# Performance work log

Hardware: AMD Instinct MI355X
Metric: run time of the kernel (lower is better)

The kernel has to match this reference:

```python
import jax, jax.numpy as jnp
import numpy as np

P, NP, EP = 10000, 50, 200      # patches, nodes/patch, edges/patch
IN, HID_E, C2, RD = 64, 256, 64, 128
HID_M, OUT, EM = 256, 16, 160000
EPS, SLOPE = 1e-5, 0.01

def lrelu(x):
    return jnp.where(x >= 0, x, SLOPE * x)

def graph_conv(x, src, dst, ew, n):
    # DGL GraphConv norm='both', bias=False, edge_weight=ew (unweighted degrees)
    ones = jnp.ones(src.shape, x.dtype)
    deg_out = jnp.maximum(jax.ops.segment_sum(ones, src, num_segments=n), 1.0)
    deg_in = jnp.maximum(jax.ops.segment_sum(ones, dst, num_segments=n), 1.0)
    h = x * jax.lax.rsqrt(deg_out)[:, None]
    agg = jax.ops.segment_sum(h[src] * ew[:, None], dst, num_segments=n)
    return agg * jax.lax.rsqrt(deg_in)[:, None]

def graph_norm(x, gamma, beta):
    # per-graph, per-channel normalization over nodes
    mu = x.mean(0, keepdims=True)
    var = x.var(0, keepdims=True)
    return gamma * (x - mu) * jax.lax.rsqrt(var + EPS) + beta

def patch_embed(feat, src, dst, ew, W1, g1, b1, W2, g2, b2, We):
    r0 = feat.mean(0)
    h = lrelu(graph_norm(graph_conv(feat, src, dst, ew, NP) @ W1, g1, b1))
    r1 = h.mean(0)
    h = lrelu(graph_norm(graph_conv(h, src, dst, ew, NP) @ W2, g2, b2))
    r2 = h.mean(0)
    return jnp.concatenate([r0, r1, r2]) @ We  # [RD]

def setup_inputs() -> dict:
    key = jax.random.key(0)
    ks = jax.random.split(key, 24)
    def kaiming(k, fi, fo):
        return jax.random.normal(k, (fi, fo), jnp.float32) * np.sqrt(2.0 / fi).astype(np.float32)
    return {
        "patch_feats": jax.random.normal(ks[0], (P, NP, IN), jnp.float32),
        "patch_src": jax.random.randint(ks[1], (P, EP), 0, NP, jnp.int32),
        "patch_dst": jax.random.randint(ks[2], (P, EP), 0, NP, jnp.int32),
        "patch_ew": jax.random.uniform(ks[3], (P, EP), jnp.float32),
        "mesh_src": jax.random.randint(ks[4], (EM,), 0, P, jnp.int32),
        "mesh_dst": jax.random.randint(ks[5], (EM,), 0, P, jnp.int32),
        "mesh_ew": jax.random.uniform(ks[6], (EM,), jnp.float32),
        "W1": kaiming(ks[7], IN, HID_E),
        "g1": 1.0 + 0.1 * jax.random.normal(ks[8], (HID_E,), jnp.float32),
        "b1": 0.1 * jax.random.normal(ks[9], (HID_E,), jnp.float32),
        "W2": kaiming(ks[10], HID_E, C2),
        "g2": 1.0 + 0.1 * jax.random.normal(ks[11], (C2,), jnp.float32),
        "b2": 0.1 * jax.random.normal(ks[12], (C2,), jnp.float32),
        "We": kaiming(ks[13], IN + HID_E + C2, RD),
        "Wc1": kaiming(ks[14], RD, HID_M),
        "g3": 1.0 + 0.1 * jax.random.normal(ks[15], (HID_M,), jnp.float32),
        "b3": 0.1 * jax.random.normal(ks[16], (HID_M,), jnp.float32),
        "Wc2": kaiming(ks[17], HID_M, HID_M),
        "g4": 1.0 + 0.1 * jax.random.normal(ks[18], (HID_M,), jnp.float32),
        "b4": 0.1 * jax.random.normal(ks[19], (HID_M,), jnp.float32),
        "Wcls": kaiming(ks[20], 2 * HID_M, OUT),
    }

def reference(patch_feats, patch_src, patch_dst, patch_ew, mesh_src, mesh_dst, mesh_ew,
              W1, g1, b1, W2, g2, b2, We, Wc1, g3, b3, Wc2, g4, b4, Wcls):
    # --- patch embedder over all patch graphs (vmapped) ---
    emb = jax.vmap(patch_embed, in_axes=(0, 0, 0, 0) + (None,) * 7)(
        patch_feats, patch_src, patch_dst, patch_ew, W1, g1, b1, W2, g2, b2, We)  # [P, RD]
    # InstanceNorm1d on 2D input == per-row normalization (no affine), then LeakyReLU
    mu = emb.mean(1, keepdims=True)
    var = emb.var(1, keepdims=True)
    emb = lrelu((emb - mu) * jax.lax.rsqrt(var + EPS))
    # --- mesh reader (single graph with P nodes) ---
    h = lrelu(graph_norm(graph_conv(emb, mesh_src, mesh_dst, mesh_ew, P) @ Wc1, g3, b3))
    ro = h.mean(0)
    h = lrelu(graph_norm(graph_conv(h, mesh_src, mesh_dst, mesh_ew, P) @ Wc2, g4, b4))
    ro = jnp.concatenate([ro, h.mean(0)])  # [2*HID_M]
    return ro[None, :] @ Wcls  # [1, OUT]
```

## Files before the change

### kernel.cpp

```cpp
#include <hip/hip_runtime.h>
#include <hip/hip_bf16.h>

#define PM    10000
#define NP_N  50
#define EP_N  200
#define EM_N  160000
#define OUT_C 16
#define EPSV  1e-5f

typedef __attribute__((ext_vector_type(8))) short short8;
typedef __attribute__((ext_vector_type(4))) float f32x4;

#define OFF_DEGO   0
#define OFF_DEGI   10016
#define OFF_OFFS   20032
#define OFF_CNT    30048
#define OFF_CUR    40064
#define OFF_CSRC   50080
#define OFF_CSRW   210080
#define OFF_STATS  370080
#define OFF_W1S    371616
#define OFF_W2S    379808
#define OFF_EMB    388000
#define OFF_AGG1   1668000
#define OFF_X1     2948000
#define OFF_HROW   5508000
#define OFF_AGG2   1668000
#define OFF_X2     4228000

__device__ __forceinline__ ushort f2bf(float f){
    __hip_bfloat16 h = __float2bfloat16(f);
    return *reinterpret_cast<ushort*>(&h);
}

__global__ __launch_bounds__(256) void prep_kernel(
    const float* __restrict__ W1, const float* __restrict__ W2,
    ushort* __restrict__ W1s, ushort* __restrict__ W2s)
{
    int gid = blockIdx.x * 256 + threadIdx.x;
    if (gid < 16384){
        int j = gid & 7, l = (gid >> 3) & 63, ki = (gid >> 9) & 1, ct = gid >> 10;
        int k = ki * 32 + ((l >> 4) << 3) + j;
        int n = ct * 16 + (l & 15);
        W1s[gid] = f2bf(W1[k * 256 + n]);
    } else {
        int g = gid - 16384;
        int j = g & 7, l = (g >> 3) & 63, ki = (g >> 9) & 7, ct = g >> 12;
        int k = ki * 32 + ((l >> 4) << 3) + j;
        int n = ct * 16 + (l & 15);
        W2s[g] = f2bf(W2[k * 64 + n]);
    }
}

__global__ __launch_bounds__(256, 4) void patch_kernel(
    const float* __restrict__ feats, const int* __restrict__ esrc,
    const int* __restrict__ edst, const float* __restrict__ eew,
    const ushort* __restrict__ W1s, const float* __restrict__ g1,
    const float* __restrict__ b1, const ushort* __restrict__ W2s,
    const float* __restrict__ g2, const float* __restrict__ b2,
    const float* __restrict__ We, float* __restrict__ embout)
{
    __shared__ __align__(16) char smem[38432];
    float*  s_A   = (float*)smem;
    char*   s_h1  = smem;
    ushort* s_fB  = (ushort*)(smem + 17408);
    ushort* s_ZB  = (ushort*)(smem + 17408);
    char*   s_G1  = smem + 25600;
    float*  s_part= (float*)(smem + 34816);
    float*  s_deg = (float*)(smem + 35840);
    float*  s_rs  = (float*)(smem + 36352);
    float*  s_r   = (float*)(smem + 36864);
    float*  s_red = (float*)(smem + 38400);

    const int tid  = threadIdx.x;
    const int p    = blockIdx.x;
    const int lane = tid & 63;
    const int wv   = tid >> 6;
    const int lnlo = lane & 15;
    const int lghi = lane >> 4;

    for (int i = tid; i < 4352; i += 256) s_A[i] = 0.f;
    for (int i = tid; i < 2048; i += 256) ((uint*)s_fB)[i] = 0u;
    if (tid < 128) s_deg[tid] = 0.f;
    int es = 0, ed = 0; float ewt = 0.f;
    if (tid < EP_N){
        es  = esrc[p * EP_N + tid];
        ed  = edst[p * EP_N + tid];
        ewt = eew[p * EP_N + tid];
    }
    __syncthreads();
    if (tid < EP_N){
        atomicAdd(&s_deg[es], 1.f);
        atomicAdd(&s_deg[64 + ed], 1.f);
        atomicAdd(&s_A[ed * 68 + es], ewt);
    }
    float4 facc = make_float4(0.f, 0.f, 0.f, 0.f);
    for (int i = tid; i < 800; i += 256){
        int s = i >> 4, cq = i & 15;
        float4 v = *(const float4*)&feats[(size_t)p * 3200 + s * 64 + cq * 4];
        facc.x += v.x; facc.y += v.y; facc.z += v.z; facc.w += v.w;
        int ki = s >> 5, ag = (s & 31) >> 3, j = s & 7;
        float vv[4] = {v.x, v.y, v.z, v.w};
        #pragma unroll
        for (int u = 0; u < 4; ++u){
            int c = cq * 4 + u;
            s_fB[(((c >> 4) * 2 + ki) * 64 + ag * 16 + (c & 15)) * 8 + j] = f2bf(vv[u]);
        }
    }
    facc.x += __shfl_xor(facc.x, 16); facc.x += __shfl_xor(facc.x, 32);
    facc.y += __shfl_xor(facc.y, 16); facc.y += __shfl_xor(facc.y, 32);
    facc.z += __shfl_xor(facc.z, 16); facc.z += __shfl_xor(facc.z, 32);
    facc.w += __shfl_xor(facc.w, 16); facc.w += __shfl_xor(facc.w, 32);
    if (lghi == 0) *(float4*)&s_part[(wv * 16 + lnlo) * 4] = facc;
    __syncthreads();
    if (tid < 128) s_rs[tid] = rsqrtf(fmaxf(s_deg[tid], 1.f));
    if (tid < 64)
        s_r[tid] = (s_part[tid] + s_part[64 + tid] + s_part[128 + tid] + s_part[192 + tid]) * 0.02f;
    __syncthreads();
    for (int i = tid; i < 4096; i += 256){
        int d = i >> 6, s = i & 63;
        s_A[d * 68 + s] *= s_rs[64 + d] * s_rs[s];
    }
    __syncthreads();
    short8 afr[4][2];
    #pragma unroll
    for (int rt = 0; rt < 4; ++rt)
        #pragma unroll
        for (int ki = 0; ki < 2; ++ki){
            int row = rt * 16 + lnlo, k0 = ki * 32 + lghi * 8;
            float4 f0 = *(const float4*)&s_A[row * 68 + k0];
            float4 f1 = *(const float4*)&s_A[row * 68 + k0 + 4];
            short8 sv;
            sv[0] = (short)f2bf(f0.x); sv[1] = (short)f2bf(f0.y);
            sv[2] = (short)f2bf(f0.z); sv[3] = (short)f2bf(f0.w);
            sv[4] = (short)f2bf(f1.x); sv[5] = (short)f2bf(f1.y);
            sv[6] = (short)f2bf(f1.z); sv[7] = (short)f2bf(f1.w);
            afr[rt][ki] = sv;
        }
    f32x4 cacc[4];
    #pragma unroll
    for (int rt = 0; rt < 4; ++rt) cacc[rt] = (f32x4){0.f, 0.f, 0.f, 0.f};
    {
        short8 fb0 = *(const short8*)&s_fB[((wv * 2 + 0) * 64 + lane) * 8];
        short8 fb1 = *(const short8*)&s_fB[((wv * 2 + 1) * 64 + lane) * 8];
        #pragma unroll
        for (int rt = 0; rt < 4; ++rt){
            cacc[rt] = __builtin_amdgcn_mfma_f32_16x16x32_bf16(afr[rt][0], fb0, cacc[rt], 0, 0, 0);
            cacc[rt] = __builtin_amdgcn_mfma_f32_16x16x32_bf16(afr[rt][1], fb1, cacc[rt], 0, 0, 0);
        }
    }
    #pragma unroll
    for (int rt = 0; rt < 4; ++rt)
        #pragma unroll
        for (int e = 0; e < 4; ++e){
            int row = rt * 16 + lghi * 4 + e;
            int col = wv * 16 + lnlo;
            *(ushort*)(s_G1 + row * 144 + ((col * 2) ^ ((row & 7) << 4))) = f2bf(cacc[rt][e]);
        }
    __syncthreads();

    f32x4 zacc[4];
    #pragma unroll
    for (int rt = 0; rt < 4; ++rt) zacc[rt] = (f32x4){0.f, 0.f, 0.f, 0.f};

    for (int h = 0; h < 2; ++h){
        short8 ga[4][2];
        #pragma unroll
        for (int rt = 0; rt < 4; ++rt)
            #pragma unroll
            for (int ki = 0; ki < 2; ++ki){
                int row = rt * 16 + lnlo, k0 = ki * 32 + lghi * 8;
                ga[rt][ki] = *(const short8*)(s_G1 + row * 144 + ((k0 * 2) ^ ((row & 7) << 4)));
            }
        #pragma unroll
        for (int ctl = 0; ctl < 2; ++ctl){
            int ctg = h * 8 + wv * 2 + ctl;
            short8 wb0 = *(const short8*)&W1s[((ctg * 2 + 0) * 64 + lane) * 8];
            short8 wb1 = *(const short8*)&W1s[((ctg * 2 + 1) * 64 + lane) * 8];
            f32x4 m[4];
            #pragma unroll
            for (int rt = 0; rt < 4; ++rt) m[rt] = (f32x4){0.f, 0.f, 0.f, 0.f};
            #pragma unroll
            for (int rt = 0; rt < 4; ++rt){
                m[rt] = __builtin_amdgcn_mfma_f32_16x16x32_bf16(ga[rt][0], wb0, m[rt], 0, 0, 0);
                m[rt] = __builtin_amdgcn_mfma_f32_16x16x32_bf16(ga[rt][1], wb1, m[rt], 0, 0, 0);
            }
            float s1 = 0.f, s2 = 0.f;
            #pragma unroll
            for (int rt = 0; rt < 4; ++rt)
                #pragma unroll
                for (int e = 0; e < 4; ++e){ float x = m[rt][e]; s1 += x; s2 += x * x; }
            s1 += __shfl_xor(s1, 16); s1 += __shfl_xor(s1, 32);
            s2 += __shfl_xor(s2, 16); s2 += __shfl_xor(s2, 32);
            float mu = s1 * 0.02f;
            float var = s2 * 0.02f - mu * mu;
            float rinv = rsqrtf(var + EPSV);
            int jg = ctg * 16 + lnlo;
            float sc = g1[jg] * rinv;
            float sh = b1[jg] - mu * sc;
            float r1p = 0.f;
            int jl = (wv * 2 + ctl) * 16 + lnlo;
            #pragma unroll
            for (int rt = 0; rt < 4; ++rt)
                #pragma unroll
                for (int e = 0; e < 4; ++e){
                    int row = rt * 16 + lghi * 4 + e;
                    float y = m[rt][e] * sc + sh;
                    float hh = (y >= 0.f) ? y : 0.01f * y;
                    hh = (row < NP_N) ? hh : 0.f;
                    r1p += hh;
                    *(ushort*)(s_h1 + row * 272 + ((jl * 2) ^ ((row & 7) << 4))) = f2bf(hh);
                }
            r1p += __shfl_xor(r1p, 16); r1p += __shfl_xor(r1p, 32);
            if (lghi == 0) s_r[64 + jg] = r1p * 0.02f;
        }
        __syncthreads();
        #pragma unroll
        for (int kil = 0; kil < 4; ++kil){
            short8 wb2 = *(const short8*)&W2s[((wv * 8 + h * 4 + kil) * 64 + lane) * 8];
            #pragma unroll
            for (int rt = 0; rt < 4; ++rt){
                int row = rt * 16 + lnlo, kl = kil * 32 + lghi * 8;
                short8 a = *(const short8*)(s_h1 + row * 272 + ((kl * 2) ^ ((row & 7) << 4)));
                zacc[rt] = __builtin_amdgcn_mfma_f32_16x16x32_bf16(a, wb2, zacc[rt], 0, 0, 0);
            }
        }
        __syncthreads();
    }

    #pragma unroll
    for (int rt = 0; rt < 4; ++rt)
        #pragma unroll
        for (int e = 0; e < 4; ++e){
            int row = rt * 16 + lghi * 4 + e;
            int ki2 = row >> 5, ag2 = (row & 31) >> 3, j2 = row & 7;
            s_ZB[((wv * 2 + ki2) * 64 + ag2 * 16 + lnlo) * 8 + j2] = f2bf(zacc[rt][e]);
        }
    __syncthreads();
    f32x4 oacc[4];
    #pragma unroll
    for (int rt = 0; rt < 4; ++rt) oacc[rt] = (f32x4){0.f, 0.f, 0.f, 0.f};
    {
        short8 zb0 = *(const short8*)&s_ZB[((wv * 2 + 0) * 64 + lane) * 8];
        short8 zb1 = *(const short8*)&s_ZB[((wv * 2 + 1) * 64 + lane) * 8];
        #pragma unroll
        for (int rt = 0; rt < 4; ++rt){
            oacc[rt] = __builtin_amdgcn_mfma_f32_16x16x32_bf16(afr[rt][0], zb0, oacc[rt], 0, 0, 0);
            oacc[rt] = __builtin_amdgcn_mfma_f32_16x16x32_bf16(afr[rt][1], zb1, oacc[rt], 0, 0, 0);
        }
    }
    {
        float s1 = 0.f, s2 = 0.f;
        #pragma unroll
        for (int rt = 0; rt < 4; ++rt)
            #pragma unroll
            for (int e = 0; e < 4; ++e){ float x = oacc[rt][e]; s1 += x; s2 += x * x; }
        s1 += __shfl_xor(s1, 16); s1 += __shfl_xor(s1, 32);
        s2 += __shfl_xor(s2, 16); s2 += __shfl_xor(s2, 32);
        float mu = s1 * 0.02f;
        float var = s2 * 0.02f - mu * mu;
        float rinv = rsqrtf(var + EPSV);
        int c2 = wv * 16 + lnlo;
        float sc = g2[c2] * rinv;
        float sh = b2[c2] - mu * sc;
        float r2p = 0.f;
        #pragma unroll
        for (int rt = 0; rt < 4; ++rt)
            #pragma unroll
            for (int e = 0; e < 4; ++e){
                int row = rt * 16 + lghi * 4 + e;
                float y = oacc[rt][e] * sc + sh;
                float hh = (y >= 0.f) ? y : 0.01f * y;
                r2p += (row < NP_N) ? hh : 0.f;
            }
        r2p += __shfl_xor(r2p, 16); r2p += __shfl_xor(r2p, 32);
        if (lghi == 0) s_r[320 + c2] = r2p * 0.02f;
    }
    __syncthreads();
    {
        int o = tid & 127, half = tid >> 7;
        float acc = 0.f;
        for (int i = half * 192; i < half * 192 + 192; ++i)
            acc = fmaf(s_r[i], We[i * 128 + o], acc);
        s_part[tid] = acc;
    }
    __syncthreads();
    float v = 0.f;
    if (tid < 128) v = s_part[tid] + s_part[tid + 128];
    float s1 = (tid < 128) ? v : 0.f;
    float s2 = s1 * s1;
    #pragma unroll
    for (int m = 32; m; m >>= 1){ s1 += __shfl_xor(s1, m); s2 += __shfl_xor(s2, m); }
    if (lane == 0 && wv < 2){ s_red[wv * 2] = s1; s_red[wv * 2 + 1] = s2; }
    __syncthreads();
    if (tid < 128){
        float T1 = s_red[0] + s_red[2], T2 = s_red[1] + s_red[3];
        float mu = T1 * (1.f / 128.f), var = T2 * (1.f / 128.f) - mu * mu;
        float y = (v - mu) * rsqrtf(var + EPSV);
        embout[(size_t)p * 128 + tid] = (y >= 0.f) ? y : 0.01f * y;
    }
}

__global__ __launch_bounds__(256) void deg_kernel(
    const int* __restrict__ msrc, const int* __restrict__ mdst,
    float* __restrict__ degO, float* __restrict__ degI, int* __restrict__ cnt)
{
    int e = blockIdx.x * 256 + threadIdx.x;
    if (e < EM_N){
        int s = msrc[e], d = mdst[e];
        atomicAdd(&degO[s], 1.f);
        atomicAdd(&degI[d], 1.f);
        atomicAdd(&cnt[d], 1);
    }
}

__global__ __launch_bounds__(256) void scan_kernel(
    const int* __restrict__ cnt, int* __restrict__ offs)
{
    __shared__ int s_sc[256];
    int t = threadIdx.x;
    int sum = 0;
    for (int k = 0; k < 40; ++k){ int i = t*40 + k; if (i < PM) sum += cnt[i]; }
    s_sc[t] = sum;
    __syncthreads();
    for (int off = 1; off < 256; off <<= 1){
        int v = (t >= off) ? s_sc[t - off] : 0;
        __syncthreads();
        s_sc[t] += v;
        __syncthreads();
    }
    int run = s_sc[t] - sum;
    for (int k = 0; k < 40; ++k){
        int i = t*40 + k;
        if (i < PM){ offs[i] = run; run += cnt[i]; }
    }
    if (t == 255) offs[PM] = s_sc[255];
}

__global__ __launch_bounds__(256) void fill_kernel(
    const int* __restrict__ msrc, const int* __restrict__ mdst,
    const float* __restrict__ mew, const float* __restrict__ degO,
    const int* __restrict__ offs, int* __restrict__ cur,
    int* __restrict__ csrc, float* __restrict__ csw)
{
    int e = blockIdx.x * 256 + threadIdx.x;
    if (e < EM_N){
        int d = mdst[e], s = msrc[e];
        int pos = atomicAdd(&cur[d], 1);
        int idx = offs[d] + pos;
        csrc[idx] = s;
        csw[idx] = mew[e] * rsqrtf(fmaxf(degO[s], 1.f));
    }
}

__global__ __launch_bounds__(256) void gather1_kernel(
    const float* __restrict__ emb, const int* __restrict__ offs,
    const int* __restrict__ csrc, const float* __restrict__ csw,
    const float* __restrict__ degI, float* __restrict__ aggT)
{
    int lane = threadIdx.x & 63, w = threadIdx.x >> 6;
    int d = blockIdx.x * 64 + lane;
    float acc[32];
    #pragma unroll
    for (int j = 0; j < 32; ++j) acc[j] = 0.f;
    if (d < PM){
        int e0 = offs[d], e1 = offs[d+1];
        for (int i = e0; i < e1; ++i){
            int s = csrc[i]; float wt = csw[i];
            const float* src = emb + (size_t)s * 128 + w * 32;
            #pragma unroll
            for (int j4 = 0; j4 < 8; ++j4){
                float4 vv = *(const float4*)(src + j4*4);
                acc[j4*4+0] = fmaf(vv.x, wt, acc[j4*4+0]);
                acc[j4*4+1] = fmaf(vv.y, wt, acc[j4*4+1]);
                acc[j4*4+2] = fmaf(vv.z, wt, acc[j4*4+2]);
                acc[j4*4+3] = fmaf(vv.w, wt, acc[j4*4+3]);
            }
        }
        float rs = rsqrtf(fmaxf(degI[d], 1.f));
        #pragma unroll
        for (int j = 0; j < 32; ++j) aggT[(size_t)(w*32 + j) * PM + d] = acc[j] * rs;
    }
}

__global__ __launch_bounds__(256) void gather2_kernel(
    const ushort* __restrict__ hRow, const int* __restrict__ offs,
    const int* __restrict__ csrc, const float* __restrict__ csw,
    const float* __restrict__ degI, float* __restrict__ aggT)
{
    int lane = threadIdx.x & 63, w = threadIdx.x >> 6;
    int d = blockIdx.x * 64 + lane;
    float acc[64];
    #pragma unroll
    for (int j = 0; j < 64; ++j) acc[j] = 0.f;
    if (d < PM){
        int e0 = offs[d], e1 = offs[d+1];
        for (int i = e0; i < e1; ++i){
            int s = csrc[i]; float wt = csw[i];
            const ushort* src = hRow + (size_t)s * 256 + w * 64;
            #pragma unroll
            for (int q4 = 0; q4 < 8; ++q4){
                uint4 qv = *(const uint4*)(src + q4*8);
                unsigned u;
                u = qv.x;
                acc[q4*8+0] = fmaf(__uint_as_float(u << 16), wt, acc[q4*8+0]);
                acc[q4*8+1] = fmaf(__uint_as_float(u & 0xffff0000u), wt, acc[q4*8+1]);
                u = qv.y;
                acc[q4*8+2] = fmaf(__uint_as_float(u << 16), wt, acc[q4*8+2]);
                acc[q4*8+3] = fmaf(__uint_as_float(u & 0xffff0000u), wt, acc[q4*8+3]);
                u = qv.z;
                acc[q4*8+4] = fmaf(__uint_as_float(u << 16), wt, acc[q4*8+4]);
                acc[q4*8+5] = fmaf(__uint_as_float(u & 0xffff0000u), wt, acc[q4*8+5]);
                u = qv.w;
                acc[q4*8+6] = fmaf(__uint_as_float(u << 16), wt, acc[q4*8+6]);
                acc[q4*8+7] = fmaf(__uint_as_float(u & 0xffff0000u), wt, acc[q4*8+7]);
            }
        }
        float rs = rsqrtf(fmaxf(degI[d], 1.f));
        #pragma unroll
        for (int j = 0; j < 64; ++j) aggT[(size_t)(w*64 + j) * PM + d] = acc[j] * rs;
    }
}

__global__ __launch_bounds__(256) void mesh_gemm_kernel(
    const float* __restrict__ AT, const float* __restrict__ W,
    float* __restrict__ XT, int K)
{
    const int tid = threadIdx.x, lane = tid & 63, wave = tid >> 6;
    const int row = blockIdx.x * 64 + lane;
    const bool act = row < PM;
    const int rowc = act ? row : (PM - 1);
    const int j0 = __builtin_amdgcn_readfirstlane((blockIdx.y * 4 + wave) * 16);
    float a[16];
    #pragma unroll
    for (int jj = 0; jj < 16; ++jj) a[jj] = 0.f;
    for (int c = 0; c < K; ++c){
        float g = AT[(size_t)c * PM + rowc];
        g = act ? g : 0.f;
        const float* wp = W + c * 256 + j0;
        #pragma unroll
        for (int jj = 0; jj < 16; ++jj) a[jj] = fmaf(g, wp[jj], a[jj]);
    }
    if (act){
        #pragma unroll
        for (int jj = 0; jj < 16; ++jj) XT[(size_t)(j0 + jj) * PM + row] = a[jj];
    }
}

__device__ __forceinline__ float block_sum2(float v1, float v2, float* s_red, float* out2)
{
    #pragma unroll
    for (int m = 32; m; m >>= 1){ v1 += __shfl_xor(v1, m); v2 += __shfl_xor(v2, m); }
    int w = threadIdx.x >> 6;
    if ((threadIdx.x & 63) == 0){ s_red[w*2] = v1; s_red[w*2+1] = v2; }
    __syncthreads();
    float t1 = s_red[0] + s_red[2] + s_red[4] + s_red[6];
    float t2 = s_red[1] + s_red[3] + s_red[5] + s_red[7];
    __syncthreads();
    *out2 = t2;
    return t1;
}

__global__ __launch_bounds__(256) void col_stats_kernel(
    const float* __restrict__ X, float* __restrict__ sums, float* __restrict__ sumsq)
{
    __shared__ float s_red[8];
    int c = blockIdx.y;
    int r = blockIdx.x * 256 + threadIdx.x;
    float v = (r < PM) ? X[(size_t)c * PM + r] : 0.f;
    float sq;
    float s = block_sum2(v, v * v, s_red, &sq);
    if (threadIdx.x == 0){ atomicAdd(&sums[c], s); atomicAdd(&sumsq[c], sq); }
}

__global__ __launch_bounds__(256) void norm1t_kernel(
    const float* __restrict__ x1T, const float* __restrict__ sums,
    const float* __restrict__ sumsq, const float* __restrict__ g,
    const float* __restrict__ b, float* __restrict__ ro, ushort* __restrict__ hRow)
{
    __shared__ float s_tile[64][65];
    int lane = threadIdx.x & 63, wvv = threadIdx.x >> 6;
    int cg = blockIdx.y;
    int rb = blockIdx.x * 64;
    int r = rb + lane;
    for (int cc = wvv; cc < 64; cc += 4){
        int c = cg * 64 + cc;
        float mu = sums[c] * (1.f / PM);
// ... 7 lines not shown
            h = (y >= 0.f) ? y : 0.01f * y;
        }
        s_tile[cc][lane] = h;
        float t = h;
        #pragma unroll
        for (int m = 32; m; m >>= 1) t += __shfl_xor(t, m);
        if (lane == 0) atomicAdd(&ro[c], t);
    }
    __syncthreads();
    for (int i = wvv; i < 64; i += 4){
        int rr = rb + i;
        if (rr < PM) hRow[(size_t)rr * 256 + cg * 64 + lane] = f2bf(s_tile[i][lane]);
    }
}

__global__ __launch_bounds__(256) void norm2_kernel(
    const float* __restrict__ X, const float* __restrict__ sums,
    const float* __restrict__ sumsq, const float* __restrict__ g,
    const float* __restrict__ b, float* __restrict__ ro)
{
    __shared__ float s_red[8];
    int c = blockIdx.y;
    int r = blockIdx.x * 256 + threadIdx.x;
    float mu = sums[c] * (1.f / PM);
    float var = sumsq[c] * (1.f / PM) - mu * mu;
    float sc = g[c] * rsqrtf(var + EPSV);
    float h = 0.f;
    if (r < PM){
        float x = X[(size_t)c * PM + r];
        float y = sc * (x - mu) + b[c];
        h = (y >= 0.f) ? y : 0.01f * y;
    }
    float dummy;
    float s = block_sum2(h, 0.f, s_red, &dummy);
    if (threadIdx.x == 0) atomicAdd(&ro[c], s);
}

__global__ __launch_bounds__(256) void final_kernel(
    const float* __restrict__ ro, const float* __restrict__ Wcls,
    float* __restrict__ out)
{
    __shared__ float s_part[256];
    int tid = threadIdx.x;
    int o = tid & 15, seg = tid >> 4;
    float pacc = 0.f;
    for (int j = seg * 32; j < seg * 32 + 32; ++j)
        pacc = fmaf(ro[j] * (1.f / PM), Wcls[j * OUT_C + o], pacc);
    s_part[tid] = pacc;
    __syncthreads();
// ... 23 lines not shown
    const float* b2    = (const float*)d_in[12];
    const float* We    = (const float*)d_in[13];
    const float* Wc1   = (const float*)d_in[14];
    const float* g3    = (const float*)d_in[15];
    const float* b3    = (const float*)d_in[16];
    const float* Wc2   = (const float*)d_in[17];
    const float* g4    = (const float*)d_in[18];
    const float* b4    = (const float*)d_in[19];
    const float* Wcls  = (const float*)d_in[20];
    float* out = (float*)d_out;
    float* ws  = (float*)d_ws;

    float*  degO  = ws + OFF_DEGO;
    float*  degI  = ws + OFF_DEGI;
    int*    offs  = (int*)(ws + OFF_OFFS);
    int*    cnt   = (int*)(ws + OFF_CNT);
    int*    cur   = (int*)(ws + OFF_CUR);
    int*    csrc  = (int*)(ws + OFF_CSRC);
    float*  csw   = ws + OFF_CSRW;
    float*  sums1 = ws + OFF_STATS;
    float*  sumsq1= ws + OFF_STATS + 256;
    float*  sums2 = ws + OFF_STATS + 512;
    float*  sumsq2= ws + OFF_STATS + 768;
    float*  ro    = ws + OFF_STATS + 1024;
    ushort* W1s   = (ushort*)(ws + OFF_W1S);
    ushort* W2s   = (ushort*)(ws + OFF_W2S);
    float*  emb   = ws + OFF_EMB;
    float*  agg1T = ws + OFF_AGG1;
    float*  x1T   = ws + OFF_X1;
    ushort* hRow  = (ushort*)(ws + OFF_HROW);
    float*  agg2T = ws + OFF_AGG2;
    float*  x2T   = ws + OFF_X2;

    hipMemsetAsync(degO, 0, 20032 * sizeof(float), stream);
    hipMemsetAsync(cnt,  0, 10016 * sizeof(int), stream);
    hipMemsetAsync(cur,  0, 10016 * sizeof(int), stream);
    hipMemsetAsync(sums1,0, 1536 * sizeof(float), stream);

    prep_kernel<<<128, 256, 0, stream>>>(W1, W2, W1s, W2s);
    patch_kernel<<<PM, 256, 0, stream>>>(feats, psrc, pdst, pew,
                                         W1s, g1, b1, W2s, g2, b2, We, emb);
    deg_kernel<<<EM_N/256, 256, 0, stream>>>(msrc, mdst, degO, degI, cnt);
    scan_kernel<<<1, 256, 0, stream>>>(cnt, offs);
    fill_kernel<<<EM_N/256, 256, 0, stream>>>(msrc, mdst, mew, degO, offs, cur, csrc, csw);
    gather1_kernel<<<157, 256, 0, stream>>>(emb, offs, csrc, csw, degI, agg1T);
    mesh_gemm_kernel<<<dim3(157, 4), 256, 0, stream>>>(agg1T, Wc1, x1T, 128);
    col_stats_kernel<<<dim3(40, 256), 256, 0, stream>>>(x1T, sums1, sumsq1);
    norm1t_kernel<<<dim3(157, 4), 256, 0, stream>>>(x1T, sums1, sumsq1, g3, b3, ro, hRow);
    gather2_kernel<<<157, 256, 0, stream>>>(hRow, offs, csrc, csw, degI, agg2T);
    mesh_gemm_kernel<<<dim3(157, 4), 256, 0, stream>>>(agg2T, Wc2, x2T, 256);
    col_stats_kernel<<<dim3(40, 256), 256, 0, stream>>>(x2T, sums2, sumsq2);
    norm2_kernel<<<dim3(40, 256), 256, 0, stream>>>(x2T, sums2, sumsq2, g4, b4, ro + 256);
    final_kernel<<<1, 256, 0, stream>>>(ro, Wcls, out);
}
```

Before: 926.6 us.

## Restructure patch kernel and fuse mesh gather, GEMM and column stats

The patch kernel now loads features straight into registers as MFMA B-fragments, folds degree normalisation into the edge atomics, and swaps the LDS round trip for Z with lane shuffles. It also drops the per-block We projection, using less shared memory so five blocks can fit per CU. The readout projection and instance norm move to a new batched emb_kernel. In the mesh stage, gather, GEMM and column-stat reduction are fused into ggemm kernels, and the separate count array is dropped in favour of the in-degree, cutting several launches and intermediate buffers. The risk is that the fused kernels run a scalar fp32 GEMM with more stat atomics, and the workspace layout now aliases more buffers.

```diff
diff --git a/kernel.cpp b/kernel.cpp
--- a/kernel.cpp
+++ b/kernel.cpp
@@ -14,23 +14,22 @@
 #define OFF_DEGO   0
 #define OFF_DEGI   10016
 #define OFF_OFFS   20032
-#define OFF_CNT    30048
-#define OFF_CUR    40064
-#define OFF_CSRC   50080
-#define OFF_CSRW   210080
-#define OFF_STATS  370080
-#define OFF_W1S    371616
-#define OFF_W2S    379808
-#define OFF_EMB    388000
-#define OFF_AGG1   1668000
-#define OFF_X1     2948000
-#define OFF_HROW   5508000
-#define OFF_AGG2   1668000
-#define OFF_X2     4228000
+#define OFF_CUR    30048
+#define OFF_CSRC   40064
+#define OFF_CSRW   200064
+#define OFF_STATS  360064
+#define OFF_W1S    361600
+#define OFF_W2S    369792
+#define OFF_RBUF   377984
+#define OFF_EMB    4217984
+#define OFF_X1T    5497984
 
 __device__ __forceinline__ ushort f2bf(float f){
     __hip_bfloat16 h = __float2bfloat16(f);
     return *reinterpret_cast<ushort*>(&h);
+}
+__device__ __forceinline__ uint pack2(float a, float b){
+    return (uint)f2bf(a) | ((uint)f2bf(b) << 16);
 }
 
 __global__ __launch_bounds__(256) void prep_kernel(
@@ -52,25 +51,21 @@
     }
 }
 
-__global__ __launch_bounds__(256, 4) void patch_kernel(
+__global__ __launch_bounds__(256, 5) void patch_kernel(
     const float* __restrict__ feats, const int* __restrict__ esrc,
     const int* __restrict__ edst, const float* __restrict__ eew,
     const ushort* __restrict__ W1s, const float* __restrict__ g1,
     const float* __restrict__ b1, const ushort* __restrict__ W2s,
     const float* __restrict__ g2, const float* __restrict__ b2,
-    const float* __restrict__ We, float* __restrict__ embout)
-{
-    __shared__ __align__(16) char smem[38432];
-    float*  s_A   = (float*)smem;
-    char*   s_h1  = smem;
-    ushort* s_fB  = (ushort*)(smem + 17408);
-    ushort* s_ZB  = (ushort*)(smem + 17408);
-    char*   s_G1  = smem + 25600;
-    float*  s_part= (float*)(smem + 34816);
-    float*  s_deg = (float*)(smem + 35840);
-    float*  s_rs  = (float*)(smem + 36352);
-    float*  s_r   = (float*)(smem + 36864);
-    float*  s_red = (float*)(smem + 38400);
+    float* __restrict__ rbuf)
+{
+    __shared__ __align__(16) char smem[29184];
+    float* s_A  = (float*)smem;
+    char*  s_h1 = smem;
+    char*  s_G1 = smem + 17408;
+    float* s_deg = (float*)(smem + 26624);
+    float* s_rs  = (float*)(smem + 27136);
+    float* s_r   = (float*)(smem + 27648);
 
     const int tid  = threadIdx.x;
     const int p    = blockIdx.x;
@@ -79,48 +74,51 @@
     const int lnlo = lane & 15;
     const int lghi = lane >> 4;
 
-    for (int i = tid; i < 4352; i += 256) s_A[i] = 0.f;
-    for (int i = tid; i < 2048; i += 256) ((uint*)s_fB)[i] = 0u;
-    if (tid < 128) s_deg[tid] = 0.f;
+    float fl[2][8];
+    {
+        const float* fbase = feats + (size_t)p * 3200 + wv * 16 + lnlo;
+        #pragma unroll
+        for (int ki = 0; ki < 2; ++ki)
+            #pragma unroll
+            for (int j = 0; j < 8; ++j){
+                int s = ki * 32 + lghi * 8 + j;
+                int sc = (s < NP_N) ? s : (NP_N - 1);
+                fl[ki][j] = fbase[sc * 64];
+            }
+    }
     int es = 0, ed = 0; float ewt = 0.f;
     if (tid < EP_N){
         es  = esrc[p * EP_N + tid];
         ed  = edst[p * EP_N + tid];
         ewt = eew[p * EP_N + tid];
     }
+    for (int i = tid; i < 1088; i += 256)
+        *(float4*)&s_A[i * 4] = make_float4(0.f, 0.f, 0.f, 0.f);
+    if (tid < 128) s_deg[tid] = 0.f;
     __syncthreads();
     if (tid < EP_N){
         atomicAdd(&s_deg[es], 1.f);
         atomicAdd(&s_deg[64 + ed], 1.f);
-        atomicAdd(&s_A[ed * 68 + es], ewt);
-    }
-    float4 facc = make_float4(0.f, 0.f, 0.f, 0.f);
-    for (int i = tid; i < 800; i += 256){
-        int s = i >> 4, cq = i & 15;
-        float4 v = *(const float4*)&feats[(size_t)p * 3200 + s * 64 + cq * 4];
-        facc.x += v.x; facc.y += v.y; facc.z += v.z; facc.w += v.w;
-        int ki = s >> 5, ag = (s & 31) >> 3, j = s & 7;
-        float vv[4] = {v.x, v.y, v.z, v.w};
-        #pragma unroll
-        for (int u = 0; u < 4; ++u){
-            int c = cq * 4 + u;
-            s_fB[(((c >> 4) * 2 + ki) * 64 + ag * 16 + (c & 15)) * 8 + j] = f2bf(vv[u]);
-        }
-    }
-    facc.x += __shfl_xor(facc.x, 16); facc.x += __shfl_xor(facc.x, 32);
-    facc.y += __shfl_xor(facc.y, 16); facc.y += __shfl_xor(facc.y, 32);
-    facc.z += __shfl_xor(facc.z, 16); facc.z += __shfl_xor(facc.z, 32);
-    facc.w += __shfl_xor(facc.w, 16); facc.w += __shfl_xor(facc.w, 32);
-    if (lghi == 0) *(float4*)&s_part[(wv * 16 + lnlo) * 4] = facc;
+    }
+    float r0s = 0.f;
+    #pragma unroll
+    for (int ki = 0; ki < 2; ++ki)
+        #pragma unroll
+        for (int j = 0; j < 8; ++j)
+            r0s += (ki * 32 + lghi * 8 + j < NP_N) ? fl[ki][j] : 0.f;
+    r0s += __shfl_xor(r0s, 16); r0s += __shfl_xor(r0s, 32);
     __syncthreads();
     if (tid < 128) s_rs[tid] = rsqrtf(fmaxf(s_deg[tid], 1.f));
-    if (tid < 64)
-        s_r[tid] = (s_part[tid] + s_part[64 + tid] + s_part[128 + tid] + s_part[192 + tid]) * 0.02f;
-    __syncthreads();
-    for (int i = tid; i < 4096; i += 256){
-        int d = i >> 6, s = i & 63;
-        s_A[d * 68 + s] *= s_rs[64 + d] * s_rs[s];
-    }
+    if (lghi == 0) s_r[wv * 16 + lnlo] = r0s * 0.02f;
+    short8 fbf[2];
+    #pragma unroll
+    for (int ki = 0; ki < 2; ++ki)
+        #pragma unroll
+        for (int j = 0; j < 8; ++j)
+            fbf[ki][j] = (short)f2bf(fl[ki][j]);
+    __syncthreads();
+    if (tid < EP_N)
+        atomicAdd(&s_A[ed * 68 + es], ewt * s_rs[es] * s_rs[64 + ed]);
     __syncthreads();
     short8 afr[4][2];
     #pragma unroll
@@ -139,15 +137,11 @@
         }
     f32x4 cacc[4];
     #pragma unroll
-    for (int rt = 0; rt < 4; ++rt) cacc[rt] = (f32x4){0.f, 0.f, 0.f, 0.f};
-    {
-        short8 fb0 = *(const short8*)&s_fB[((wv * 2 + 0) * 64 + lane) * 8];
-        short8 fb1 = *(const short8*)&s_fB[((wv * 2 + 1) * 64 + lane) * 8];
-        #pragma unroll
-        for (int rt = 0; rt < 4; ++rt){
-            cacc[rt] = __builtin_amdgcn_mfma_f32_16x16x32_bf16(afr[rt][0], fb0, cacc[rt], 0, 0, 0);
-            cacc[rt] = __builtin_amdgcn_mfma_f32_16x16x32_bf16(afr[rt][1], fb1, cacc[rt], 0, 0, 0);
-        }
+    for (int rt = 0; rt < 4; ++rt) cacc[rt] = (f32x4){0.f,0.f,0.f,0.f};
+    #pragma unroll
+    for (int rt = 0; rt < 4; ++rt){
+        cacc[rt] = __builtin_amdgcn_mfma_f32_16x16x32_bf16(afr[rt][0], fbf[0], cacc[rt], 0,0,0);
+        cacc[rt] = __builtin_amdgcn_mfma_f32_16x16x32_bf16(afr[rt][1], fbf[1], cacc[rt], 0,0,0);
     }
     #pragma unroll
     for (int rt = 0; rt < 4; ++rt)
@@ -155,13 +149,13 @@
         for (int e = 0; e < 4; ++e){
             int row = rt * 16 + lghi * 4 + e;
             int col = wv * 16 + lnlo;
-            *(ushort*)(s_G1 + row * 144 + ((col * 2) ^ ((row & 7) << 4))) = f2bf(cacc[rt][e]);
+            *(ushort*)(s_G1 + row * 144 + ((col * 2) ^ ((row & 8) << 2))) = f2bf(cacc[rt][e]);
         }
     __syncthreads();
 
     f32x4 zacc[4];
     #pragma unroll
-    for (int rt = 0; rt < 4; ++rt) zacc[rt] = (f32x4){0.f, 0.f, 0.f, 0.f};
+    for (int rt = 0; rt < 4; ++rt) zacc[rt] = (f32x4){0.f,0.f,0.f,0.f};
 
     for (int h = 0; h < 2; ++h){
         short8 ga[4][2];
@@ -170,7 +164,7 @@
             #pragma unroll
             for (int ki = 0; ki < 2; ++ki){
                 int row = rt * 16 + lnlo, k0 = ki * 32 + lghi * 8;
-                ga[rt][ki] = *(const short8*)(s_G1 + row * 144 + ((k0 * 2) ^ ((row & 7) << 4)));
+                ga[rt][ki] = *(const short8*)(s_G1 + row * 144 + ((k0 * 2) ^ ((row & 8) << 2)));
             }
         #pragma unroll
         for (int ctl = 0; ctl < 2; ++ctl){
@@ -179,17 +173,17 @@
             short8 wb1 = *(const short8*)&W1s[((ctg * 2 + 1) * 64 + lane) * 8];
             f32x4 m[4];
             #pragma unroll
-            for (int rt = 0; rt < 4; ++rt) m[rt] = (f32x4){0.f, 0.f, 0.f, 0.f};
+            for (int rt = 0; rt < 4; ++rt) m[rt] = (f32x4){0.f,0.f,0.f,0.f};
             #pragma unroll
             for (int rt = 0; rt < 4; ++rt){
-                m[rt] = __builtin_amdgcn_mfma_f32_16x16x32_bf16(ga[rt][0], wb0, m[rt], 0, 0, 0);
-                m[rt] = __builtin_amdgcn_mfma_f32_16x16x32_bf16(ga[rt][1], wb1, m[rt], 0, 0, 0);
+                m[rt] = __builtin_amdgcn_mfma_f32_16x16x32_bf16(ga[rt][0], wb0, m[rt], 0,0,0);
+                m[rt] = __builtin_amdgcn_mfma_f32_16x16x32_bf16(ga[rt][1], wb1, m[rt], 0,0,0);
             }
             float s1 = 0.f, s2 = 0.f;
             #pragma unroll
             for (int rt = 0; rt < 4; ++rt)
                 #pragma unroll
-                for (int e = 0; e < 4; ++e){ float x = m[rt][e]; s1 += x; s2 += x * x; }
+                for (int e = 0; e < 4; ++e){ float x = m[rt][e]; s1 += x; s2 += x*x; }
             s1 += __shfl_xor(s1, 16); s1 += __shfl_xor(s1, 32);
             s2 += __shfl_xor(s2, 16); s2 += __shfl_xor(s2, 32);
             float mu = s1 * 0.02f;
@@ -209,7 +203,7 @@
                     float hh = (y >= 0.f) ? y : 0.01f * y;
                     hh = (row < NP_N) ? hh : 0.f;
                     r1p += hh;
-                    *(ushort*)(s_h1 + row * 272 + ((jl * 2) ^ ((row & 7) << 4))) = f2bf(hh);
+                    *(ushort*)(s_h1 + row * 272 + ((jl * 2) ^ ((row & 8) << 2))) = f2bf(hh);
                 }
             r1p += __shfl_xor(r1p, 16); r1p += __shfl_xor(r1p, 32);
             if (lghi == 0) s_r[64 + jg] = r1p * 0.02f;
@@ -221,40 +215,52 @@
             #pragma unroll
             for (int rt = 0; rt < 4; ++rt){
                 int row = rt * 16 + lnlo, kl = kil * 32 + lghi * 8;
-                short8 a = *(const short8*)(s_h1 + row * 272 + ((kl * 2) ^ ((row & 7) << 4)));
-                zacc[rt] = __builtin_amdgcn_mfma_f32_16x16x32_bf16(a, wb2, zacc[rt], 0, 0, 0);
+                short8 a = *(const short8*)(s_h1 + row * 272 + ((kl * 2) ^ ((row & 8) << 2)));
+                zacc[rt] = __builtin_amdgcn_mfma_f32_16x16x32_bf16(a, wb2, zacc[rt], 0,0,0);
             }
         }
         __syncthreads();
     }
 
-    #pragma unroll
-    for (int rt = 0; rt < 4; ++rt)
-        #pragma unroll
-        for (int e = 0; e < 4; ++e){
-            int row = rt * 16 + lghi * 4 + e;
-            int ki2 = row >> 5, ag2 = (row & 31) >> 3, j2 = row & 7;
-            s_ZB[((wv * 2 + ki2) * 64 + ag2 * 16 + lnlo) * 8 + j2] = f2bf(zacc[rt][e]);
-        }
-    __syncthreads();
+    uint pk[4][2];
+    #pragma unroll
+    for (int rt = 0; rt < 4; ++rt){
+        pk[rt][0] = pack2(zacc[rt][0], zacc[rt][1]);
+        pk[rt][1] = pack2(zacc[rt][2], zacc[rt][3]);
+    }
+    bool hi = (lghi >= 2);
+    int lane_lo = (((lghi * 2 + 0) & 3) << 4) + lnlo;
+    int lane_hi = (((lghi * 2 + 1) & 3) << 4) + lnlo;
+    short8 zb[2];
+    #pragma unroll
+    for (int ki = 0; ki < 2; ++ki){
+        uint sA = hi ? pk[ki*2+1][0] : pk[ki*2][0];
+        uint sB = hi ? pk[ki*2+1][1] : pk[ki*2][1];
+        uint w0 = (uint)__shfl((int)sA, lane_lo, 64);
+        uint w1 = (uint)__shfl((int)sB, lane_lo, 64);
+        uint w2 = (uint)__shfl((int)sA, lane_hi, 64);
+        uint w3 = (uint)__shfl((int)sB, lane_hi, 64);
+        short8 z;
+        z[0] = (short)(w0 & 0xffff); z[1] = (short)(w0 >> 16);
+        z[2] = (short)(w1 & 0xffff); z[3] = (short)(w1 >> 16);
+        z[4] = (short)(w2 & 0xffff); z[5] = (short)(w2 >> 16);
+        z[6] = (short)(w3 & 0xffff); z[7] = (short)(w3 >> 16);
+        zb[ki] = z;
+    }
     f32x4 oacc[4];
     #pragma unroll
-    for (int rt = 0; rt < 4; ++rt) oacc[rt] = (f32x4){0.f, 0.f, 0.f, 0.f};
-    {
-        short8 zb0 = *(const short8*)&s_ZB[((wv * 2 + 0) * 64 + lane) * 8];
-        short8 zb1 = *(const short8*)&s_ZB[((wv * 2 + 1) * 64 + lane) * 8];
-        #pragma unroll
-        for (int rt = 0; rt < 4; ++rt){
-            oacc[rt] = __builtin_amdgcn_mfma_f32_16x16x32_bf16(afr[rt][0], zb0, oacc[rt], 0, 0, 0);
-            oacc[rt] = __builtin_amdgcn_mfma_f32_16x16x32_bf16(afr[rt][1], zb1, oacc[rt], 0, 0, 0);
-        }
+    for (int rt = 0; rt < 4; ++rt) oacc[rt] = (f32x4){0.f,0.f,0.f,0.f};
+    #pragma unroll
+    for (int rt = 0; rt < 4; ++rt){
+        oacc[rt] = __builtin_amdgcn_mfma_f32_16x16x32_bf16(afr[rt][0], zb[0], oacc[rt], 0,0,0);
+        oacc[rt] = __builtin_amdgcn_mfma_f32_16x16x32_bf16(afr[rt][1], zb[1], oacc[rt], 0,0,0);
     }
     {
         float s1 = 0.f, s2 = 0.f;
         #pragma unroll
         for (int rt = 0; rt < 4; ++rt)
             #pragma unroll
-            for (int e = 0; e < 4; ++e){ float x = oacc[rt][e]; s1 += x; s2 += x * x; }
+            for (int e = 0; e < 4; ++e){ float x = oacc[rt][e]; s1 += x; s2 += x*x; }
         s1 += __shfl_xor(s1, 16); s1 += __shfl_xor(s1, 32);
         s2 += __shfl_xor(s2, 16); s2 += __shfl_xor(s2, 32);
         float mu = s1 * 0.02f;
@@ -277,50 +283,72 @@
         if (lghi == 0) s_r[320 + c2] = r2p * 0.02f;
     }
     __syncthreads();
-    {
-        int o = tid & 127, half = tid >> 7;
-        float acc = 0.f;
-        for (int i = half * 192; i < half * 192 + 192; ++i)
-            acc = fmaf(s_r[i], We[i * 128 + o], acc);
-        s_part[tid] = acc;
-    }
-    __syncthreads();
-    float v = 0.f;
-    if (tid < 128) v = s_part[tid] + s_part[tid + 128];
-    float s1 = (tid < 128) ? v : 0.f;
-    float s2 = s1 * s1;
-    #pragma unroll
-    for (int m = 32; m; m >>= 1){ s1 += __shfl_xor(s1, m); s2 += __shfl_xor(s2, m); }
-    if (lane == 0 && wv < 2){ s_red[wv * 2] = s1; s_red[wv * 2 + 1] = s2; }
-    __syncthreads();
-    if (tid < 128){
-        float T1 = s_red[0] + s_red[2], T2 = s_red[1] + s_red[3];
-        float mu = T1 * (1.f / 128.f), var = T2 * (1.f / 128.f) - mu * mu;
-        float y = (v - mu) * rsqrtf(var + EPSV);
-        embout[(size_t)p * 128 + tid] = (y >= 0.f) ? y : 0.01f * y;
-    }
+    if (tid < 96)
+        *(float4*)&rbuf[(size_t)p * 384 + tid * 4] = *(const float4*)&s_r[tid * 4];
+}
+
+__global__ __launch_bounds__(256) void emb_kernel(
+    const float* __restrict__ rbuf, const float* __restrict__ We,
+    float* __restrict__ emb)
+{
+    __shared__ float s_R[16 * 388];
+    int tid = threadIdx.x;
+    int rb = blockIdx.x * 16;
+    for (int i = tid; i < 1536; i += 256){
+        int r = i / 96, q = i - r * 96;
+        *(float4*)&s_R[r * 388 + q * 4] =
+            *(const float4*)&rbuf[(size_t)(rb + r) * 384 + q * 4];
+    }
+    __syncthreads();
+    int r = tid >> 4, c0 = (tid & 15) * 8;
+    float acc[8];
+    #pragma unroll
+    for (int j = 0; j < 8; ++j) acc[j] = 0.f;
+    for (int k = 0; k < 384; ++k){
+        float a = s_R[r * 388 + k];
+        const float* wp = &We[k * 128 + c0];
+        #pragma unroll
+        for (int j = 0; j < 8; ++j) acc[j] = fmaf(a, wp[j], acc[j]);
+    }
+    float s1 = 0.f, s2 = 0.f;
+    #pragma unroll
+    for (int j = 0; j < 8; ++j){ s1 += acc[j]; s2 += acc[j] * acc[j]; }
+    s1 += __shfl_xor(s1, 1); s2 += __shfl_xor(s2, 1);
+    s1 += __shfl_xor(s1, 2); s2 += __shfl_xor(s2, 2);
+    s1 += __shfl_xor(s1, 4); s2 += __shfl_xor(s2, 4);
+    s1 += __shfl_xor(s1, 8); s2 += __shfl_xor(s2, 8);
+    float mu = s1 * (1.f / 128.f);
+    float var = s2 * (1.f / 128.f) - mu * mu;
+    float rinv = rsqrtf(var + EPSV);
+    float o[8];
+    #pragma unroll
+    for (int j = 0; j < 8; ++j){
+        float y = (acc[j] - mu) * rinv;
+        o[j] = (y >= 0.f) ? y : 0.01f * y;
+    }
+    float* op = &emb[(size_t)(rb + r) * 128 + c0];
+    *(float4*)op = make_float4(o[0], o[1], o[2], o[3]);
+    *(float4*)(op + 4) = make_float4(o[4], o[5], o[6], o[7]);
 }
 
 __global__ __launch_bounds__(256) void deg_kernel(
     const int* __restrict__ msrc, const int* __restrict__ mdst,
-    float* __restrict__ degO, float* __restrict__ degI, int* __restrict__ cnt)
+    float* __restrict__ degO, float* __restrict__ degI)
 {
     int e = blockIdx.x * 256 + threadIdx.x;
     if (e < EM_N){
-        int s = msrc[e], d = mdst[e];
-        atomicAdd(&degO[s], 1.f);
-        atomicAdd(&degI[d], 1.f);
-        atomicAdd(&cnt[d], 1);
+        atomicAdd(&degO[msrc[e]], 1.f);
+        atomicAdd(&degI[mdst[e]], 1.f);
     }
 }
 
 __global__ __launch_bounds__(256) void scan_kernel(
-    const int* __restrict__ cnt, int* __restrict__ offs)
+    const float* __restrict__ degI, int* __restrict__ offs)
 {
     __shared__ int s_sc[256];
     int t = threadIdx.x;
     int sum = 0;
-    for (int k = 0; k < 40; ++k){ int i = t*40 + k; if (i < PM) sum += cnt[i]; }
+    for (int k = 0; k < 40; ++k){ int i = t * 40 + k; if (i < PM) sum += (int)degI[i]; }
     s_sc[t] = sum;
     __syncthreads();
     for (int off = 1; off < 256; off <<= 1){
@@ -331,8 +359,8 @@
     }
     int run = s_sc[t] - sum;
     for (int k = 0; k < 40; ++k){
-        int i = t*40 + k;
-        if (i < PM){ offs[i] = run; run += cnt[i]; }
+        int i = t * 40 + k;
+        if (i < PM){ offs[i] = run; run += (int)degI[i]; }
     }
     if (t == 255) offs[PM] = s_sc[255];
 }
@@ -353,124 +381,65 @@
     }
 }
 
-__global__ __launch_bounds__(256) void gather1_kernel(
+__global__ __launch_bounds__(256) void ggemm1_kernel(
     const float* __restrict__ emb, const int* __restrict__ offs,
     const int* __restrict__ csrc, const float* __restrict__ csw,
-    const float* __restrict__ degI, float* __restrict__ aggT)
-{
-    int lane = threadIdx.x & 63, w = threadIdx.x >> 6;
-    int d = blockIdx.x * 64 + lane;
-    float acc[32];
-    #pragma unroll
-    for (int j = 0; j < 32; ++j) acc[j] = 0.f;
-    if (d < PM){
-        int e0 = offs[d], e1 = offs[d+1];
-        for (int i = e0; i < e1; ++i){
-            int s = csrc[i]; float wt = csw[i];
-            const float* src = emb + (size_t)s * 128 + w * 32;
-            #pragma unroll
-            for (int j4 = 0; j4 < 8; ++j4){
-                float4 vv = *(const float4*)(src + j4*4);
-                acc[j4*4+0] = fmaf(vv.x, wt, acc[j4*4+0]);
-                acc[j4*4+1] = fmaf(vv.y, wt, acc[j4*4+1]);
-                acc[j4*4+2] = fmaf(vv.z, wt, acc[j4*4+2]);
-                acc[j4*4+3] = fmaf(vv.w, wt, acc[j4*4+3]);
-            }
+    const float* __restrict__ degI, const float* __restrict__ Wc1,
+    float* __restrict__ x1T, float* __restrict__ sums, float* __restrict__ sumsq)
+{
+    __shared__ float s_agg[16 * 132];
+    int tid = threadIdx.x, lane = tid & 63, w = tid >> 6;
+    for (int i = 0; i < 4; ++i){
+        int li = w * 4 + i;
+        int d = blockIdx.x * 16 + li;
+        int e0 = offs[d], e1 = offs[d + 1];
+        float a0 = 0.f, a1 = 0.f;
+        int e = e0;
+        for (; e + 1 < e1; e += 2){
+            int sA = csrc[e], sB = csrc[e + 1];
+            float wA = csw[e], wB = csw[e + 1];
+            float2 vA = *(const float2*)&emb[(size_t)sA * 128 + lane * 2];
+            float2 vB = *(const float2*)&emb[(size_t)sB * 128 + lane * 2];
+            a0 = fmaf(vA.x, wA, a0); a1 = fmaf(vA.y, wA, a1);
+            a0 = fmaf(vB.x, wB, a0); a1 = fmaf(vB.y, wB, a1);
+        }
+        if (e < e1){
+            int sA = csrc[e]; float wA = csw[e];
+            float2 vA = *(const float2*)&emb[(size_t)sA * 128 + lane * 2];
+            a0 = fmaf(vA.x, wA, a0); a1 = fmaf(vA.y, wA, a1);
         }
         float rs = rsqrtf(fmaxf(degI[d], 1.f));
-        #pragma unroll
-        for (int j = 0; j < 32; ++j) aggT[(size_t)(w*32 + j) * PM + d] = acc[j] * rs;
-    }
-}
-
-__global__ __launch_bounds__(256) void gather2_kernel(
-    const ushort* __restrict__ hRow, const int* __restrict__ offs,
-    const int* __restrict__ csrc, const float* __restrict__ csw,
-    const float* __restrict__ degI, float* __restrict__ aggT)
-{
-    int lane = threadIdx.x & 63, w = threadIdx.x >> 6;
-    int d = blockIdx.x * 64 + lane;
-    float acc[64];
-    #pragma unroll
-    for (int j = 0; j < 64; ++j) acc[j] = 0.f;
-    if (d < PM){
-        int e0 = offs[d], e1 = offs[d+1];
-        for (int i = e0; i < e1; ++i){
-            int s = csrc[i]; float wt = csw[i];
-            const ushort* src = hRow + (size_t)s * 256 + w * 64;
-            #pragma unroll
-            for (int q4 = 0; q4 < 8; ++q4){
-                uint4 qv = *(const uint4*)(src + q4*8);
-                unsigned u;
-                u = qv.x;
-                acc[q4*8+0] = fmaf(__uint_as_float(u << 16), wt, acc[q4*8+0]);
-                acc[q4*8+1] = fmaf(__uint_as_float(u & 0xffff0000u), wt, acc[q4*8+1]);
-                u = qv.y;
-                acc[q4*8+2] = fmaf(__uint_as_float(u << 16), wt, acc[q4*8+2]);
-                acc[q4*8+3] = fmaf(__uint_as_float(u & 0xffff0000u), wt, acc[q4*8+3]);
-                u = qv.z;
-                acc[q4*8+4] = fmaf(__uint_as_float(u << 16), wt, acc[q4*8+4]);
-                acc[q4*8+5] = fmaf(__uint_as_float(u & 0xffff0000u), wt, acc[q4*8+5]);
-                u = qv.w;
-                acc[q4*8+6] = fmaf(__uint_as_float(u << 16), wt, acc[q4*8+6]);
-                acc[q4*8+7] = fmaf(__uint_as_float(u & 0xffff0000u), wt, acc[q4*8+7]);
-            }
-        }
-        float rs = rsqrtf(fmaxf(degI[d], 1.f));
-        #pragma unroll
-        for (int j = 0; j < 64; ++j) aggT[(size_t)(w*64 + j) * PM + d] = acc[j] * rs;
-    }
-}
-
-__global__ __launch_bounds__(256) void mesh_gemm_kernel(
-    const float* __restrict__ AT, const float* __restrict__ W,
-    float* __restrict__ XT, int K)
-{
-    const int tid = threadIdx.x, lane = tid & 63, wave = tid >> 6;
-    const int row = blockIdx.x * 64 + lane;
-    const bool act = row < PM;
-    const int rowc = act ? row : (PM - 1);
-    const int j0 = __builtin_amdgcn_readfirstlane((blockIdx.y * 4 + wave) * 16);
-    float a[16];
-    #pragma unroll
-    for (int jj = 0; jj < 16; ++jj) a[jj] = 0.f;
-    for (int c = 0; c < K; ++c){
-        float g = AT[(size_t)c * PM + rowc];
-        g = act ? g : 0.f;
-        const float* wp = W + c * 256 + j0;
-        #pragma unroll
-        for (int jj = 0; jj < 16; ++jj) a[jj] = fmaf(g, wp[jj], a[jj]);
-    }
-    if (act){
-        #pragma unroll
-        for (int jj = 0; jj < 16; ++jj) XT[(size_t)(j0 + jj) * PM + row] = a[jj];
-    }
-}
-
-__device__ __forceinline__ float block_sum2(float v1, float v2, float* s_red, float* out2)
-{
-    #pragma unroll
-    for (int m = 32; m; m >>= 1){ v1 += __shfl_xor(v1, m); v2 += __shfl_xor(v2, m); }
-    int w = threadIdx.x >> 6;
-    if ((threadIdx.x & 63) == 0){ s_red[w*2] = v1; s_red[w*2+1] = v2; }
-    __syncthreads();
-    float t1 = s_red[0] + s_red[2] + s_red[4] + s_red[6];
-    float t2 = s_red[1] + s_red[3] + s_red[5] + s_red[7];
-    __syncthreads();
-    *out2 = t2;
-    return t1;
-}
-
-__global__ __launch_bounds__(256) void col_stats_kernel(
-    const float* __restrict__ X, float* __restrict__ sums, float* __restrict__ sumsq)
-{
-    __shared__ float s_red[8];
-    int c = blockIdx.y;
-    int r = blockIdx.x * 256 + threadIdx.x;
-    float v = (r < PM) ? X[(size_t)c * PM + r] : 0.f;
-    float sq;
-    float s = block_sum2(v, v * v, s_red, &sq);
-    if (threadIdx.x == 0){ atomicAdd(&sums[c], s); atomicAdd(&sumsq[c], sq); }
+        s_agg[li * 132 + lane * 2]     = a0 * rs;
+        s_agg[li * 132 + lane * 2 + 1] = a1 * rs;
+    }
+    __syncthreads();
+    int r = lane & 15, cg = lane >> 4;
+    int c0 = w * 64 + cg * 16;
+    float acc[16];
+    #pragma unroll
+    for (int jj = 0; jj < 16; ++jj) acc[jj] = 0.f;
+    #pragma unroll 2
+    for (int k = 0; k < 128; ++k){
+        float a = s_agg[r * 132 + k];
+        const float* wp = &Wc1[k * 256 + c0];
+        #pragma unroll
+        for (int jj = 0; jj < 16; ++jj) acc[jj] = fmaf(a, wp[jj], acc[jj]);
+    }
+    int row = blockIdx.x * 16 + r;
+    #pragma unroll
+    for (int jj = 0; jj < 16; ++jj) x1T[(size_t)(c0 + jj) * PM + row] = acc[jj];
+    #pragma unroll
+    for (int jj = 0; jj < 16; ++jj){
+        float s1 = acc[jj], s2 = acc[jj] * acc[jj];
+        s1 += __shfl_xor(s1, 1); s2 += __shfl_xor(s2, 1);
+        s1 += __shfl_xor(s1, 2); s2 += __shfl_xor(s2, 2);
+        s1 += __shfl_xor(s1, 4); s2 += __shfl_xor(s2, 4);
+        s1 += __shfl_xor(s1, 8); s2 += __shfl_xor(s2, 8);
+        if (r == 0){
+            atomicAdd(&sums[c0 + jj], s1);
+            atomicAdd(&sumsq[c0 + jj], s2);
+        }
+    }
 }
 
 __global__ __launch_bounds__(256) void norm1t_kernel(
@@ -508,12 +477,79 @@
     }
 }
 
+__global__ __launch_bounds__(256) void ggemm2_kernel(
+    const ushort* __restrict__ hRow, const int* __restrict__ offs,
+    const int* __restrict__ csrc, const float* __restrict__ csw,
+    const float* __restrict__ degI, const float* __restrict__ Wc2,
+    float* __restrict__ x2T, float* __restrict__ sums, float* __restrict__ sumsq)
+{
+    __shared__ float s_agg[16 * 260];
+    int tid = threadIdx.x, lane = tid & 63, w = tid >> 6;
+    for (int i = 0; i < 4; ++i){
+        int li = w * 4 + i;
+        int d = blockIdx.x * 16 + li;
+        int e0 = offs[d], e1 = offs[d + 1];
+        float a0 = 0.f, a1 = 0.f, a2 = 0.f, a3 = 0.f;
+        for (int e = e0; e < e1; ++e){
+            int s = csrc[e]; float wt = csw[e];
+            uint2 qv = *(const uint2*)&hRow[(size_t)s * 256 + lane * 4];
+            a0 = fmaf(__uint_as_float(qv.x << 16), wt, a0);
+            a1 = fmaf(__uint_as_float(qv.x & 0xffff0000u), wt, a1);
+            a2 = fmaf(__uint_as_float(qv.y << 16), wt, a2);
+            a3 = fmaf(__uint_as_float(qv.y & 0xffff0000u), wt, a3);
+        }
+        float rs = rsqrtf(fmaxf(degI[d], 1.f));
+        *(float4*)&s_agg[li * 260 + lane * 4] =
+            make_float4(a0 * rs, a1 * rs, a2 * rs, a3 * rs);
+    }
+    __syncthreads();
+    int r = lane & 15, cg = lane >> 4;
+    int c0 = w * 64 + cg * 16;
+    float acc[16];
+    #pragma unroll
+    for (int jj = 0; jj < 16; ++jj) acc[jj] = 0.f;
+    #pragma unroll 2
+    for (int k = 0; k < 256; ++k){
+        float a = s_agg[r * 260 + k];
+        const float* wp = &Wc2[k * 256 + c0];
+        #pragma unroll
+        for (int jj = 0; jj < 16; ++jj) acc[jj] = fmaf(a, wp[jj], acc[jj]);
+    }
+    int row = blockIdx.x * 16 + r;
+    #pragma unroll
+    for (int jj = 0; jj < 16; ++jj) x2T[(size_t)(c0 + jj) * PM + row] = acc[jj];
+    #pragma unroll
+    for (int jj = 0; jj < 16; ++jj){
+        float s1 = acc[jj], s2 = acc[jj] * acc[jj];
+        s1 += __shfl_xor(s1, 1); s2 += __shfl_xor(s2, 1);
+        s1 += __shfl_xor(s1, 2); s2 += __shfl_xor(s2, 2);
+        s1 += __shfl_xor(s1, 4); s2 += __shfl_xor(s2, 4);
+        s1 += __shfl_xor(s1, 8); s2 += __shfl_xor(s2, 8);
+        if (r == 0){
+            atomicAdd(&sums[c0 + jj], s1);
+            atomicAdd(&sumsq[c0 + jj], s2);
+        }
+    }
+}
+
+__device__ __forceinline__ float block_sum1(float v1, float* s_red)
+{
+    #pragma unroll
+    for (int m = 32; m; m >>= 1) v1 += __shfl_xor(v1, m);
+    int w = threadIdx.x >> 6;
+    if ((threadIdx.x & 63) == 0) s_red[w] = v1;
+    __syncthreads();
+    float t1 = s_red[0] + s_red[1] + s_red[2] + s_red[3];
+    __syncthreads();
+    return t1;
+}
+
 __global__ __launch_bounds__(256) void norm2_kernel(
     const float* __restrict__ X, const float* __restrict__ sums,
     const float* __restrict__ sumsq, const float* __restrict__ g,
     const float* __restrict__ b, float* __restrict__ ro)
 {
-    __shared__ float s_red[8];
+    __shared__ float s_red[4];
     int c = blockIdx.y;
     int r = blockIdx.x * 256 + threadIdx.x;
     float mu = sums[c] * (1.f / PM);
@@ -525,8 +561,7 @@
         float y = sc * (x - mu) + b[c];
         h = (y >= 0.f) ? y : 0.01f * y;
     }
-    float dummy;
-    float s = block_sum2(h, 0.f, s_red, &dummy);
+    float s = block_sum1(h, s_red);
     if (threadIdx.x == 0) atomicAdd(&ro[c], s);
 }
 
@@ -580,7 +615,6 @@
     float*  degO  = ws + OFF_DEGO;
     float*  degI  = ws + OFF_DEGI;
     int*    offs  = (int*)(ws + OFF_OFFS);
-    int*    cnt   = (int*)(ws + OFF_CNT);
     int*    cur   = (int*)(ws + OFF_CUR);
     int*    csrc  = (int*)(ws + OFF_CSRC);
     float*  csw   = ws + OFF_CSRW;
@@ -591,31 +625,28 @@
     float*  ro    = ws + OFF_STATS + 1024;
     ushort* W1s   = (ushort*)(ws + OFF_W1S);
     ushort* W2s   = (ushort*)(ws + OFF_W2S);
+    float*  rbuf  = ws + OFF_RBUF;
+    ushort* hRow  = (ushort*)(ws + OFF_RBUF);
     float*  emb   = ws + OFF_EMB;
-    float*  agg1T = ws + OFF_AGG1;
-    float*  x1T   = ws + OFF_X1;
-    ushort* hRow  = (ushort*)(ws + OFF_HROW);
-    float*  agg2T = ws + OFF_AGG2;
-    float*  x2T   = ws + OFF_X2;
+    float*  x1T   = ws + OFF_X1T;
+    float*  x2T   = ws + OFF_X1T;
 
     hipMemsetAsync(degO, 0, 20032 * sizeof(float), stream);
-    hipMemsetAsync(cnt,  0, 10016 * sizeof(int), stream);
     hipMemsetAsync(cur,  0, 10016 * sizeof(int), stream);
     hipMemsetAsync(sums1,0, 1536 * sizeof(float), stream);
 
     prep_kernel<<<128, 256, 0, stream>>>(W1, W2, W1s, W2s);
     patch_kernel<<<PM, 256, 0, stream>>>(feats, psrc, pdst, pew,
-                                         W1s, g1, b1, W2s, g2, b2, We, emb);
-    deg_kernel<<<EM_N/256, 256, 0, stream>>>(msrc, mdst, degO, degI, cnt);
-    scan_kernel<<<1, 256, 0, stream>>>(cnt, offs);
+                                         W1s, g1, b1, W2s, g2, b2, rbuf);
+    emb_kernel<<<625, 256, 0, stream>>>(rbuf, We, emb);
+    deg_kernel<<<EM_N/256, 256, 0, stream>>>(msrc, mdst, degO, degI);
+    scan_kernel<<<1, 256, 0, stream>>>(degI, offs);
     fill_kernel<<<EM_N/256, 256, 0, stream>>>(msrc, mdst, mew, degO, offs, cur, csrc, csw);
-    gather1_kernel<<<157, 256, 0, stream>>>(emb, offs, csrc, csw, degI, agg1T);
-    mesh_gemm_kernel<<<dim3(157, 4), 256, 0, stream>>>(agg1T, Wc1, x1T, 128);
-    col_stats_kernel<<<dim3(40, 256), 256, 0, stream>>>(x1T, sums1, sumsq1);
+    ggemm1_kernel<<<625, 256, 0, stream>>>(emb, offs, csrc, csw, degI, Wc1,
+                                           x1T, sums1, sumsq1);
     norm1t_kernel<<<dim3(157, 4), 256, 0, stream>>>(x1T, sums1, sumsq1, g3, b3, ro, hRow);
-    gather2_kernel<<<157, 256, 0, stream>>>(hRow, offs, csrc, csw, degI, agg2T);
-    mesh_gemm_kernel<<<dim3(157, 4), 256, 0, stream>>>(agg2T, Wc2, x2T, 256);
-    col_stats_kernel<<<dim3(40, 256), 256, 0, stream>>>(x2T, sums2, sumsq2);
+    ggemm2_kernel<<<625, 256, 0, stream>>>(hRow, offs, csrc, csw, degI, Wc2,
+                                           x2T, sums2, sumsq2);
     norm2_kernel<<<dim3(40, 256), 256, 0, stream>>>(x2T, sums2, sumsq2, g4, b4, ro + 256);
     final_kernel<<<1, 256, 0, stream>>>(ro, Wcls, out);
 }
```

After: 1.303 ms. +40.6%, slower.
